# Performance work log

Hardware: AMD Instinct MI355X
Metric: run time of the kernel (lower is better)

## Reference

```python
import jax, jax.numpy as jnp
import numpy as np
import math

DIM = 896
NH = 8
HD = DIM // NH  # 112
B, T, KA_RAW, KT = 64, 8, 64, 512
KA = KA_RAW + 1  # adapter tokens + p conditioning token


def rope_cos_sin(L, hd):
    inv = 1.0 / (10000.0 ** (jnp.arange(0, hd, 2, dtype=jnp.float32) / hd))
    freqs = jnp.arange(L, dtype=jnp.float32)[:, None] * inv[None, :]  # (L, hd/2)
    emb = jnp.concatenate([freqs, freqs], axis=-1)  # (L, hd)
    return jnp.cos(emb), jnp.sin(emb)


def rotate_half(x):
    # interleaved rotation, faithful to the torch code
    x1 = x[..., ::2]
    x2 = x[..., 1::2]
    return jnp.stack((-x2, x1), axis=-1).reshape(x.shape)


def rope_apply(t, cos, sin):
    # cos/sin: (L, hd) broadcast over (B, H, L, hd)
    return t * cos + rotate_half(t) * sin


def heads(t):
    Bb, L, _ = t.shape
    return t.reshape(Bb, L, NH, HD).transpose(0, 2, 1, 3)  # (B, H, L, hd)


def setup_inputs() -> dict:
    key = jax.random.key(0)
    ks = jax.random.split(key, 32)
    s = 0.02
    d = {
        'x': jax.random.normal(ks[0], (B, T, DIM), jnp.float32),
        'h_a': jax.random.normal(ks[1], (B, KA_RAW, DIM), jnp.float32),
        'h_t': jax.random.normal(ks[2], (B, KT, DIM), jnp.float32),
        'p': jax.random.normal(ks[3], (B, 1, DIM), jnp.float32),
    }
    names = ['Wq', 'Wks', 'Wvs', 'Wka', 'Wva', 'Wkt', 'Wvt', 'Wo', 'Wf']
    for i, n in enumerate(names):
        d[n] = s * jax.random.normal(ks[4 + i], (DIM, DIM), jnp.float32)
        d['b' + n[1:]] = s * jax.random.normal(ks[16 + i], (DIM,), jnp.float32)
    d['gate'] = jnp.full((1,), 0.1, jnp.float32)  # nonzero so task branch is active
    d['ln_g'] = jnp.ones((DIM,), jnp.float32)
    d['ln_b'] = jnp.zeros((DIM,), jnp.float32)
    return d


def reference(x, h_a, h_t, p,
              Wq, bq, Wks, bks, Wvs, bvs, Wka, bka, Wva, bva,
              Wkt, bkt, Wvt, bvt, Wo, bo, Wf, bf,
              gate, ln_g, ln_b):
    ratio_g = jnp.tanh(gate)  # (1,)
    h_ad = jnp.concatenate([h_a, p], axis=1)  # (B, KA, C)

    q = heads(x @ Wq + bq)            # (B,H,T,hd)
    k_s = heads(x @ Wks + bks)
    v_s = heads(x @ Wvs + bvs)
    k_a = heads(h_ad @ Wka + bka)     # (B,H,KA,hd)
    v_a = heads(h_ad @ Wva + bva)
    k_t = heads(h_t @ Wkt + bkt)      # (B,H,KT,hd)
    v_t = heads(h_t @ Wvt + bvt)

    cos_m, sin_m = rope_cos_sin(T, HD)
    q = rope_apply(q, cos_m, sin_m)
    k_s = rope_apply(k_s, cos_m, sin_m)
    cos_a, sin_a = rope_cos_sin(KA, HD)
    k_a = rope_apply(k_a, cos_a, sin_a)
    cos_t, sin_t = rope_cos_sin(KT, HD)
    k_t = rope_apply(k_t, cos_t, sin_t)

    s_self = jnp.einsum('bhtd,bhkd->bhtk', q, k_s)
    s_ad = jnp.einsum('bhtd,bhkd->bhtk', q, k_a)
    s_task = jnp.einsum('bhtd,bhkd->bhtk', q, k_t) * ratio_g
    scores = jnp.concatenate([s_self, s_ad, s_task], axis=-1) / math.sqrt(HD)
    w = jax.nn.softmax(scores, axis=-1)  # (B,H,T,T+KA+KT)

    v = jnp.concatenate([v_s, v_a, v_t], axis=2)  # (B,H,T+KA+KT,hd)
    out = jnp.einsum('bhtk,bhkd->bhtd', w, v)
    out = out.transpose(0, 2, 1, 3).reshape(x.shape)  # (B,T,C)
    out = out @ Wo + bo

    y = out + x
    mu = jnp.mean(y, axis=-1, keepdims=True)
    var = jnp.var(y, axis=-1, keepdims=True)
    yn = (y - mu) / jnp.sqrt(var + 1e-5) * ln_g + ln_b
    return jax.nn.relu(yn @ Wf + bf)
```

## Files before the change

kernel.cpp:

```cpp
#include <hip/hip_runtime.h>
#include <hip/hip_bf16.h>
#include <math.h>

#define DIM 896
#define DD  (DIM * DIM)
#define NH 8
#define HD 112
#define BB 64
#define TT 8
#define KA 65
#define KAPAD 4224
#define KT 512
#define NKEYS (TT + KA + KT)

#define EPI_NONE  0
#define EPI_ROPE  1
#define EPI_RESID 2
#define EPI_RELU  3

#define NEG_L2_10K_OVER_56 (-0.2373327285062406f)

#ifndef __has_builtin
#define __has_builtin(x) 0
#endif
#if __has_builtin(__builtin_amdgcn_global_load_lds)
#define HAS_GLL 1
#else
#define HAS_GLL 0
#endif

typedef __attribute__((ext_vector_type(8))) short bf16x8_t;
typedef __attribute__((ext_vector_type(4))) float f32x4_t;

__device__ __forceinline__ short f2bf(float f) {
  unsigned u = __float_as_uint(f);
  u += 0x7fffu + ((u >> 16) & 1u);
  return (short)(u >> 16);
}
__device__ __forceinline__ float bf2f(short s) {
  return __uint_as_float(((unsigned)(unsigned short)s) << 16);
}
__device__ __forceinline__ unsigned cvt_pk_bf16(float lo, float hi) {
  unsigned r;
  asm("v_cvt_pk_bf16_f32 %0, %1, %2" : "=v"(r) : "v"(lo), "v"(hi));
  return r;
}
__device__ __forceinline__ void gll16(const short* g, short* lbase, int lane) {
#if HAS_GLL
  __builtin_amdgcn_global_load_lds(
      (const __attribute__((address_space(1))) unsigned*)g,
      (__attribute__((address_space(3))) unsigned*)lbase, 16, 0, 0);
#else
  *(bf16x8_t*)(lbase + lane * 8) = *(const bf16x8_t*)g;
#endif
}

struct W9 { const float* w[9]; };

__global__ __launch_bounds__(256) void wtrans(W9 ws, short* __restrict__ Wt)
{
  __shared__ float t[32][33];
  const float* W = ws.w[blockIdx.z];
  short* dst = Wt + (size_t)blockIdx.z * DD;
  const int bx = blockIdx.x, by = blockIdx.y;
  const int tx = threadIdx.x & 31, ty = threadIdx.x >> 5;
#pragma unroll
  for (int i = 0; i < 4; ++i)
    t[ty + i * 8][tx] = W[(size_t)(by * 32 + ty + i * 8) * DIM + bx * 32 + tx];
  __syncthreads();
#pragma unroll
  for (int i = 0; i < 4; ++i)
    dst[(size_t)(bx * 32 + ty + i * 8) * DIM + by * 32 + tx] = f2bf(t[tx][ty + i * 8]);
}

__global__ __launch_bounds__(256) void build_had(
    const float* __restrict__ h_a, const float* __restrict__ p,
    short* __restrict__ had)
{
  const int i = blockIdx.x * 256 + threadIdx.x;
  const int total = KAPAD * DIM / 8;
  if (i >= total) return;
  const int c = (i % 112) * 8;
  const int row = i / 112;
  bf16x8_t o;
  if (row >= BB * KA) {
#pragma unroll
    for (int j = 0; j < 8; ++j) o[j] = 0;
  } else {
    const int b = row / KA, j = row % KA;
    const float* src = (j < KA - 1) ? h_a + ((size_t)b * (KA - 1) + j) * DIM + c
                                    : p + (size_t)b * DIM + c;
    const float4 a = *(const float4*)src;
    const float4 d = *(const float4*)(src + 4);
    o[0] = f2bf(a.x); o[1] = f2bf(a.y); o[2] = f2bf(a.z); o[3] = f2bf(a.w);
    o[4] = f2bf(d.x); o[5] = f2bf(d.y); o[6] = f2bf(d.z); o[7] = f2bf(d.w);
  }
  ((bf16x8_t*)had)[i] = o;
}

struct EpiCfg {
  const float* bias[3];
  float* outF[3];
  short* outB[3];
  const float* resid;
  int epi[3];
  int pos_mod[3];
  int row_off;
  int hm[3];
  int hm_L[3];
  int hm_ltot[3];
  int swz;
};

template <bool AF32, bool DOLN>
__device__ __forceinline__ void gemm_body(
    short* As, short* Bs,
    const short* A, const float* Af, const short* Wt,
    const EpiCfg& cfg, int bx, int by,
    const float* smu, const float* srs,
    const float* lngam, const float* lnbet)
{
  const int tid = threadIdx.x;
  const int wave = tid >> 6, lane = tid & 63;
  const int sub = bx / 7;
  const int col0 = (bx % 7) * 128;
  const int row0 = by * 128;
  const int wm = wave >> 1, wn = wave & 1;
  const int lm = lane & 15, lq = lane >> 4;

  const int sr = lane >> 3;
  const int sg = (lane & 7) ^ sr;
  const short* Wg = Wt + (size_t)(sub * DIM + col0 + wave * 32 + sr) * DIM + sg * 8;
  const short* Ag = nullptr;
  if constexpr (!AF32)
    Ag = A + (size_t)(row0 + wave * 32 + sr) * DIM + sg * 8;

  f32x4_t acc[4][4];
#pragma unroll
  for (int i = 0; i < 4; ++i)
#pragma unroll
    for (int j = 0; j < 4; ++j) acc[i][j] = (f32x4_t){0.f, 0.f, 0.f, 0.f};

  for (int k0 = 0; k0 < DIM; k0 += 64) {
    __syncthreads();
    if constexpr (AF32) {
#pragma unroll
      for (int j = 0; j < 4; ++j) {
        const int c = tid + 256 * j;
        const int row = c >> 3, g = c & 7;
        const float* srcp = Af + (size_t)(row0 + row) * DIM + k0 + g * 8;
        const float4 a0 = *(const float4*)srcp;
        const float4 a1 = *(const float4*)(srcp + 4);
        float e[8] = {a0.x, a0.y, a0.z, a0.w, a1.x, a1.y, a1.z, a1.w};
        if constexpr (DOLN) {
          const float mu = smu[row], rs = srs[row];
#pragma unroll
          for (int q = 0; q < 8; ++q) {
            const int k = k0 + g * 8 + q;
            e[q] = (e[q] - mu) * rs * lngam[k] + lnbet[k];
          }
        }
        uint4 w;
        w.x = cvt_pk_bf16(e[0], e[1]); w.y = cvt_pk_bf16(e[2], e[3]);
        w.z = cvt_pk_bf16(e[4], e[5]); w.w = cvt_pk_bf16(e[6], e[7]);
        *(uint4*)&As[row * 64 + ((g ^ (row & 7)) << 3)] = w;
      }
    } else {
#pragma unroll
      for (int j = 0; j < 4; ++j)
        gll16(Ag + (size_t)(j * 8) * DIM + k0, &As[(wave * 32 + j * 8) * 64], lane);
    }
#pragma unroll
    for (int j = 0; j < 4; ++j)
      gll16(Wg + (size_t)(j * 8) * DIM + k0, &Bs[(wave * 32 + j * 8) * 64], lane);
    __syncthreads();

    bf16x8_t afr[4][2], bfr[4][2];
#pragma unroll
    for (int t = 0; t < 4; ++t) {
      const int ra = wm * 64 + t * 16 + lm;
      const int rb = wn * 64 + t * 16 + lm;
      afr[t][0] = *(const bf16x8_t*)&As[ra * 64 + (((lq) ^ (ra & 7)) << 3)];
      afr[t][1] = *(const bf16x8_t*)&As[ra * 64 + (((4 + lq) ^ (ra & 7)) << 3)];
      bfr[t][0] = *(const bf16x8_t*)&Bs[rb * 64 + (((lq) ^ (rb & 7)) << 3)];
      bfr[t][1] = *(const bf16x8_t*)&Bs[rb * 64 + (((4 + lq) ^ (rb & 7)) << 3)];
    }
#pragma unroll
    for (int kk = 0; kk < 2; ++kk)
#pragma unroll
      for (int tm = 0; tm < 4; ++tm)
#pragma unroll
        for (int tn = 0; tn < 4; ++tn)
          acc[tm][tn] = __builtin_amdgcn_mfma_f32_16x16x32_bf16(
              afr[tm][kk], bfr[tn][kk], acc[tm][tn], 0, 0, 0);
  }

  const float* bias = cfg.bias[sub];
  float* outF = cfg.outF[sub];
  short* outB = cfg.outB[sub];
  const int epi = cfg.epi[sub], pm = cfg.pos_mod[sub];
  const int hm = cfg.hm[sub];
  const int L = cfg.hm_L[sub], ltot = cfg.hm_ltot[sub];

  if (hm) {
    int gl[4][4];
#pragma unroll
    for (int tm = 0; tm < 4; ++tm) {
      const int g = cfg.row_off + row0 + wm * 64 + tm * 16 + lq * 4;
      int bq2 = g / L;
      int l = g - bq2 * L;
#pragma unroll
      for (int r = 0; r < 4; ++r) {
        gl[tm][r] = l;
        if (++l == L) { l = 0; ++bq2; }
      }
    }
    short* Cs = As;
    __syncthreads();
#pragma unroll
    for (int tn = 0; tn < 4; ++tn) {
      const int lc = wn * 64 + tn * 16 + lm;
      const int col = col0 + lc;
      const float bv = bias[col];
      float fr = 0.f, sgn = 0.f;
      if (epi == EPI_ROPE) {
        const int d0 = col % HD;
        fr = exp2f((float)(d0 % 56) * NEG_L2_10K_OVER_56);
        sgn = (d0 & 1) ? 1.f : -1.f;
      }
#pragma unroll
      for (int tm = 0; tm < 4; ++tm) {
#pragma unroll
        for (int r = 0; r < 4; ++r) {
          float v = acc[tm][tn][r] + bv;
          if (epi == EPI_ROPE) {
            const float prt = __shfl_xor(v, 1);
            float s, c;
            __sincosf((float)gl[tm][r] * fr, &s, &c);
            v = v * c + sgn * prt * s;
          }
          const int lr = wm * 64 + tm * 16 + lq * 4 + r;
          const int gp = (lc >> 3) ^ (((lr >> 2) & 3) << 1);
          Cs[lr * 128 + gp * 8 + (lc & 7)] = f2bf(v);
        }
      }
    }
    __syncthreads();
#pragma unroll
    for (int i = 0; i < 8; ++i) {
      const int ch = tid + 256 * i;
      const int lr = ch >> 4, g = ch & 15;
      const int phys = g ^ (((lr >> 2) & 3) << 1);
      const bf16x8_t val = *(const bf16x8_t*)&Cs[lr * 128 + phys * 8];
      const int grow = cfg.row_off + row0 + lr;
      const int bq2 = grow / L;
      const int l = grow - bq2 * L;
      const int col = col0 + g * 8;
      const int h = col / HD, d = col - h * HD;
      if (bq2 < BB)
        *(bf16x8_t*)&outB[((size_t)(bq2 * NH + h) * ltot + l) * HD + d] = val;
    }
    return;
  }

#pragma unroll
  for (int tn = 0; tn < 4; ++tn) {
    const int col = col0 + wn * 64 + tn * 16 + lm;
    const float bv = bias[col];
#pragma unroll
    for (int tm = 0; tm < 4; ++tm) {
#pragma unroll
      for (int r = 0; r < 4; ++r) {
        const int grow = cfg.row_off + row0 + wm * 64 + tm * 16 + lq * 4 + r;
        float v = acc[tm][tn][r] + bv;
        if (epi == EPI_RESID) {
          v += cfg.resid[(size_t)grow * DIM + col];
        } else if (epi == EPI_RELU) {
          v = fmaxf(v, 0.f);
        }
        if (outB) outB[(size_t)grow * DIM + col] = f2bf(v);
        else      outF[(size_t)grow * DIM + col] = v;
      }
    }
  }
}

template <bool AF32>
__global__ __launch_bounds__(256) void gemm_bf16(
    const short* __restrict__ A, const float* __restrict__ Af,
    const short* __restrict__ Wt, EpiCfg cfg)
{
  __shared__ __align__(16) short lds[2 * 128 * 64];
  int bx = blockIdx.x, by = blockIdx.y;
  if (cfg.swz) {
    const int nx = gridDim.x;
    const int bid = blockIdx.x + blockIdx.y * nx;
    const int xcd = bid & 7, ixd = bid >> 3;
    const int rpx = gridDim.y >> 3;
    bx = ixd % nx;
    by = xcd * rpx + ixd / nx;
  }
  gemm_body<AF32, false>(lds, lds + 128 * 64, A, Af, Wt, cfg, bx, by,
                         nullptr, nullptr, nullptr, nullptr);
}

__global__ __launch_bounds__(256) void gemm_ffn(
    const float* __restrict__ Y, const float* __restrict__ lng,
    const float* __restrict__ lnb, const short* __restrict__ Wt, EpiCfg cfg)
{
  __shared__ __align__(16) short lds[2 * 128 * 64];
  __shared__ float glds[DIM], blds[DIM];
  __shared__ float smu[128], srs[128];
  const int tid = threadIdx.x;
  const int row0 = blockIdx.y * 128;
  for (int i = tid; i < DIM; i += 256) { glds[i] = lng[i]; blds[i] = lnb[i]; }
  {
    const int r = tid >> 1, h = tid & 1;
    const float* rp = Y + (size_t)(row0 + r) * DIM + h * 448;
    float s = 0.f, q = 0.f;
    for (int i = 0; i < 448; i += 4) {
      const float4 v = *(const float4*)(rp + i);
      s += v.x + v.y + v.z + v.w;
      q = fmaf(v.x, v.x, fmaf(v.y, v.y, fmaf(v.z, v.z, fmaf(v.w, v.w, q))));
    }
    s += __shfl_xor(s, 1);
    q += __shfl_xor(q, 1);
    if (h == 0) {
      const float mu = s * (1.f / DIM);
      const float var = q * (1.f / DIM) - mu * mu;
      smu[r] = mu;
      srs[r] = 1.f / sqrtf(var + 1e-5f);
    }
  }
  __syncthreads();
  gemm_body<true, true>(lds, lds + 128 * 64, nullptr, Y, Wt, cfg,
                        blockIdx.x, blockIdx.y, smu, srs, glds, blds);
}

#define SCP 10

__global__ __launch_bounds__(1024, 8) void attn_kernel(
    const short* __restrict__ q, const short* __restrict__ kall,
    const short* __restrict__ vall, const float* __restrict__ gate,
    short* __restrict__ out)
{
  __shared__ __align__(16) float qs[TT * HD];
  __shared__ __align__(16) float sc[NKEYS * SCP];
  __shared__ float red[TT * TT * HD];
  __shared__ float isum[TT];
  const int tid = threadIdx.x;
  const int bh = blockIdx.x;
  const float scale = 0.09449111825230681f;
  const float rg = tanhf(gate[0]);

  if (tid < TT * HD) qs[tid] = bf2f(q[(size_t)bh * (TT * HD) + tid]);
  __syncthreads();

  if (tid < NKEYS) {
    const int k = tid;
    const short* kp = kall + ((size_t)bh * NKEYS + k) * HD;
    float dot[TT] = {};
    for (int d8 = 0; d8 < HD; d8 += 8) {
      const bf16x8_t kv8 = *(const bf16x8_t*)(kp + d8);
      float kf[8];
#pragma unroll
      for (int j = 0; j < 8; ++j) kf[j] = bf2f(kv8[j]);
#pragma unroll
      for (int t = 0; t < TT; ++t) {
        const float4 qa = *(const float4*)&qs[t * HD + d8];
        const float4 qb4 = *(const float4*)&qs[t * HD + d8 + 4];
        dot[t] = fmaf(qa.x, kf[0], dot[t]);
        dot[t] = fmaf(qa.y, kf[1], dot[t]);
        dot[t] = fmaf(qa.z, kf[2], dot[t]);
        dot[t] = fmaf(qa.w, kf[3], dot[t]);
        dot[t] = fmaf(qb4.x, kf[4], dot[t]);
        dot[t] = fmaf(qb4.y, kf[5], dot[t]);
        dot[t] = fmaf(qb4.z, kf[6], dot[t]);
        dot[t] = fmaf(qb4.w, kf[7], dot[t]);
      }
    }
    const float s = (k >= TT + KA) ? scale * rg : scale;
#pragma unroll
    for (int t = 0; t < TT; ++t) sc[k * SCP + t] = dot[t] * s;
  }
  __syncthreads();

  const int wave = tid >> 6, lane = tid & 63;
  if (wave < TT) {
    const int t = wave;
    float m = -1e30f;
    for (int k = lane; k < NKEYS; k += 64) m = fmaxf(m, sc[k * SCP + t]);
#pragma unroll
    for (int o = 32; o >= 1; o >>= 1) m = fmaxf(m, __shfl_xor(m, o));
    float sum = 0.f;
    for (int k = lane; k < NKEYS; k += 64) {
      const float e = expf(sc[k * SCP + t] - m);
      sc[k * SCP + t] = e;
      sum += e;
    }
#pragma unroll
    for (int o = 32; o >= 1; o >>= 1) sum += __shfl_xor(sum, o);
    if (lane == 0) isum[t] = 1.f / sum;
  }
  __syncthreads();

  if (tid < TT * HD) {
    const int g = tid / HD, d = tid - (tid / HD) * HD;
    const int kb = (g * NKEYS) / TT, ke = ((g + 1) * NKEYS) / TT;
    const short* vp = vall + (size_t)bh * (NKEYS * HD) + d;
    float acc[TT] = {};
    for (int k = kb; k < ke; ++k) {
      const float vv = bf2f(vp[(size_t)k * HD]);
      const float2 s0 = *(const float2*)&sc[k * SCP];
      const float2 s1 = *(const float2*)&sc[k * SCP + 2];
      const float2 s2 = *(const float2*)&sc[k * SCP + 4];
      const float2 s3 = *(const float2*)&sc[k * SCP + 6];
      acc[0] = fmaf(s0.x, vv, acc[0]);
      acc[1] = fmaf(s0.y, vv, acc[1]);
      acc[2] = fmaf(s1.x, vv, acc[2]);
      acc[3] = fmaf(s1.y, vv, acc[3]);
      acc[4] = fmaf(s2.x, vv, acc[4]);
      acc[5] = fmaf(s2.y, vv, acc[5]);
      acc[6] = fmaf(s3.x, vv, acc[6]);
      acc[7] = fmaf(s3.y, vv, acc[7]);
    }
#pragma unroll
    for (int t = 0; t < TT; ++t) red[(g * TT + t) * HD + d] = acc[t];
  }
  __syncthreads();

  if (tid < TT * HD) {
    const int t = tid / HD, d = tid - (tid / HD) * HD;
    float a = 0.f;
#pragma unroll
    for (int g = 0; g < TT; ++g) a += red[(g * TT + t) * HD + d];
    out[((size_t)(bh >> 3) * TT + t) * DIM + (bh & 7) * HD + d] = f2bf(a * isum[t]);
  }
}

extern "C" void kernel_launch(void* const* d_in, const int* in_sizes, int n_in,
                              void* d_out, int out_size, void* d_ws, size_t ws_size,
                              hipStream_t stream)
{
  const float* x   = (const float*)d_in[0];
  const float* h_a = (const float*)d_in[1];
  const float* h_t = (const float*)d_in[2];
  const float* p   = (const float*)d_in[3];
  const float* Wq  = (const float*)d_in[4];  const float* bq  = (const float*)d_in[5];
  const float* Wks = (const float*)d_in[6];  const float* bks = (const float*)d_in[7];
  const float* Wvs = (const float*)d_in[8];  const float* bvs = (const float*)d_in[9];
  const float* Wka = (const float*)d_in[10]; const float* bka = (const float*)d_in[11];
  const float* Wva = (const float*)d_in[12]; const float* bva = (const float*)d_in[13];
  const float* Wkt = (const float*)d_in[14]; const float* bkt = (const float*)d_in[15];
  const float* Wvt = (const float*)d_in[16]; const float* bvt = (const float*)d_in[17];
  const float* Wo  = (const float*)d_in[18]; const float* bo  = (const float*)d_in[19];
  const float* Wf  = (const float*)d_in[20]; const float* bf_ = (const float*)d_in[21];
  const float* gate = (const float*)d_in[22];
  const float* ln_g = (const float*)d_in[23];
  const float* ln_b = (const float*)d_in[24];

  const size_t SZ_HAD = (size_t)KAPAD * DIM * 2;
  const size_t SZ_SM  = (size_t)BB * TT * DIM * 2;
  const size_t SZ_KV  = (size_t)BB * NH * NKEYS * HD * 2;
  const size_t SZ_WT  = (size_t)9 * DD * 2;
  const size_t needed = SZ_HAD + SZ_SM * 2 + SZ_KV * 2 + SZ_WT
                        + (size_t)BB * TT * DIM * 4;
  if (ws_size < needed) return;

  char* wsp = (char*)d_ws;
  short* hadb = (short*)wsp; wsp += SZ_HAD;
  short* qb   = (short*)wsp; wsp += SZ_SM;
  short* kall = (short*)wsp; wsp += SZ_KV;
  short* vall = (short*)wsp; wsp += SZ_KV;
  short* WtA  = (short*)wsp; wsp += SZ_WT;
  short* attn_outb = (short*)wsp; wsp += SZ_SM;
  float* yb   = (float*)wsp; wsp += (size_t)BB * TT * DIM * 4;

  dim3 blk(256);

  W9 w9; const float* Ws[9] = {Wq, Wks, Wvs, Wka, Wva, Wkt, Wvt, Wo, Wf};
  for (int i = 0; i < 9; ++i) w9.w[i] = Ws[i];
  wtrans<<<dim3(28, 28, 9), blk, 0, stream>>>(w9, WtA);

  build_had<<<(KAPAD * DIM / 8 + 255) / 256, blk, 0, stream>>>(h_a, p, hadb);

  {
    EpiCfg c = {};
    c.bias[0] = bq;  c.outB[0] = qb;   c.epi[0] = EPI_ROPE; c.pos_mod[0] = TT;
    c.hm[0] = 1; c.hm_L[0] = TT; c.hm_ltot[0] = TT;
    c.bias[1] = bks; c.outB[1] = kall; c.epi[1] = EPI_ROPE; c.pos_mod[1] = TT;
    c.hm[1] = 1; c.hm_L[1] = TT; c.hm_ltot[1] = NKEYS;
    c.bias[2] = bvs; c.outB[2] = vall; c.epi[2] = EPI_NONE; c.pos_mod[2] = 1;
    c.hm[2] = 1; c.hm_L[2] = TT; c.hm_ltot[2] = NKEYS;
    gemm_bf16<true><<<dim3(21, BB * TT / 128), blk, 0, stream>>>(nullptr, x, WtA, c);
  }
  {
    EpiCfg c = {};
    c.bias[0] = bka; c.outB[0] = kall + (size_t)TT * HD; c.epi[0] = EPI_ROPE;
    c.pos_mod[0] = KA; c.hm[0] = 1; c.hm_L[0] = KA; c.hm_ltot[0] = NKEYS;
    c.bias[1] = bva; c.outB[1] = vall + (size_t)TT * HD; c.epi[1] = EPI_NONE;
    c.pos_mod[1] = 1; c.hm[1] = 1; c.hm_L[1] = KA; c.hm_ltot[1] = NKEYS;
    gemm_bf16<false><<<dim3(14, KAPAD / 128), blk, 0, stream>>>(
        hadb, nullptr, WtA + (size_t)3 * DD, c);
  }
  {
    EpiCfg c = {};
    c.bias[0] = bkt; c.outB[0] = kall + (size_t)(TT + KA) * HD; c.epi[0] = EPI_ROPE;
    c.pos_mod[0] = KT; c.hm[0] = 1; c.hm_L[0] = KT; c.hm_ltot[0] = NKEYS;
    c.bias[1] = bvt; c.outB[1] = vall + (size_t)(TT + KA) * HD; c.epi[1] = EPI_NONE;
    c.pos_mod[1] = 1; c.hm[1] = 1; c.hm_L[1] = KT; c.hm_ltot[1] = NKEYS;
    c.row_off = 0;
    c.swz = 1;
    gemm_bf16<true><<<dim3(14, BB * KT / 128), blk, 0, stream>>>(
        nullptr, h_t, WtA + (size_t)5 * DD, c);
  }

  attn_kernel<<<BB * NH, dim3(1024), 0, stream>>>(qb, kall, vall, gate, attn_outb);

  {
    EpiCfg c = {};
    c.bias[0] = bo; c.outF[0] = yb; c.epi[0] = EPI_RESID; c.pos_mod[0] = 1;
    c.resid = x;
    gemm_bf16<false><<<dim3(7, BB * TT / 128), blk, 0, stream>>>(
        attn_outb, nullptr, WtA + (size_t)7 * DD, c);
  }
  {
    EpiCfg c = {};
    c.bias[0] = bf_; c.outF[0] = (float*)d_out; c.epi[0] = EPI_RELU; c.pos_mod[0] = 1;
    gemm_ffn<<<dim3(7, BB * TT / 128), blk, 0, stream>>>(
        yb, ln_g, ln_b, WtA + (size_t)8 * DD, c);
  }
}
```

Baseline: 695.9 us.

## Add software-pipelined GEMM with register-prefetched fp32 A and triple-buffered weights

Adds a new gemm_t kernel for the fp32-input projections (QKV self and task K/V). It prefetches fp32 A tiles into registers two steps ahead, converts them to bf16 into double-buffered LDS, and triple-buffers weight tiles via async global-to-LDS loads. It uses explicit vmcnt waits and a single barrier per k-step. The goal is to overlap global loads with MFMA work and remove the two-barrier serial load/compute loop, at the cost of more LDS (80KB) and register pressure, which may lower occupancy.

```diff
diff --git a/kernel.cpp b/kernel.cpp
--- a/kernel.cpp
+++ b/kernel.cpp
@@ -112,6 +112,215 @@
   int swz;
 };
 
+__device__ __forceinline__ void compute_step(
+    const short* As, const short* Bs, f32x4_t (&acc)[4][4],
+    int wm, int wn, int lm, int lq)
+{
+  bf16x8_t afr[4][2], bfr[4][2];
+#pragma unroll
+  for (int t = 0; t < 4; ++t) {
+    const int ra = wm * 64 + t * 16 + lm;
+    const int rb = wn * 64 + t * 16 + lm;
+    afr[t][0] = *(const bf16x8_t*)&As[ra * 64 + (((lq) ^ (ra & 7)) << 3)];
+    afr[t][1] = *(const bf16x8_t*)&As[ra * 64 + (((4 + lq) ^ (ra & 7)) << 3)];
+    bfr[t][0] = *(const bf16x8_t*)&Bs[rb * 64 + (((lq) ^ (rb & 7)) << 3)];
+    bfr[t][1] = *(const bf16x8_t*)&Bs[rb * 64 + (((4 + lq) ^ (rb & 7)) << 3)];
+  }
+#pragma unroll
+  for (int kk = 0; kk < 2; ++kk)
+#pragma unroll
+    for (int tm = 0; tm < 4; ++tm)
+#pragma unroll
+      for (int tn = 0; tn < 4; ++tn)
+        acc[tm][tn] = __builtin_amdgcn_mfma_f32_16x16x32_bf16(
+            afr[tm][kk], bfr[tn][kk], acc[tm][tn], 0, 0, 0);
+}
+
+__device__ __forceinline__ void epilogue_hm(
+    short* Cs, f32x4_t (&acc)[4][4], const EpiCfg& cfg,
+    int bx, int by, int wm, int wn, int lm, int lq, int tid)
+{
+  const int sub = bx / 7;
+  const int col0 = (bx % 7) * 128;
+  const int row0 = by * 128;
+  const float* bias = cfg.bias[sub];
+  short* outB = cfg.outB[sub];
+  const int epi = cfg.epi[sub];
+  const int L = cfg.hm_L[sub], ltot = cfg.hm_ltot[sub];
+  int gl[4][4];
+#pragma unroll
+  for (int tm = 0; tm < 4; ++tm) {
+    const int g = cfg.row_off + row0 + wm * 64 + tm * 16 + lq * 4;
+    int bq2 = g / L;
+    int l = g - bq2 * L;
+#pragma unroll
+    for (int r = 0; r < 4; ++r) {
+      gl[tm][r] = l;
+      if (++l == L) { l = 0; ++bq2; }
+    }
+  }
+  __syncthreads();
+#pragma unroll
+  for (int tn = 0; tn < 4; ++tn) {
+    const int lc = wn * 64 + tn * 16 + lm;
+    const int col = col0 + lc;
+    const float bv = bias[col];
+    float fr = 0.f, sgn = 0.f;
+    if (epi == EPI_ROPE) {
+      const int d0 = col % HD;
+      fr = exp2f((float)(d0 % 56) * NEG_L2_10K_OVER_56);
+      sgn = (d0 & 1) ? 1.f : -1.f;
+    }
+#pragma unroll
+    for (int tm = 0; tm < 4; ++tm) {
+#pragma unroll
+      for (int r = 0; r < 4; ++r) {
+        float v = acc[tm][tn][r] + bv;
+        if (epi == EPI_ROPE) {
+          const float prt = __shfl_xor(v, 1);
+          float s, c;
+          __sincosf((float)gl[tm][r] * fr, &s, &c);
+          v = v * c + sgn * prt * s;
+        }
+        const int lr = wm * 64 + tm * 16 + lq * 4 + r;
+        const int gp = (lc >> 3) ^ (((lr >> 2) & 3) << 1);
+        Cs[lr * 128 + gp * 8 + (lc & 7)] = f2bf(v);
+      }
+    }
+  }
+  __syncthreads();
+#pragma unroll
+  for (int i = 0; i < 8; ++i) {
+    const int ch = tid + 256 * i;
+    const int lr = ch >> 4, g = ch & 15;
+    const int phys = g ^ (((lr >> 2) & 3) << 1);
+    const bf16x8_t val = *(const bf16x8_t*)&Cs[lr * 128 + phys * 8];
+    const int grow = cfg.row_off + row0 + lr;
+    const int bq2 = grow / L;
+    const int l = grow - bq2 * L;
+    const int col = col0 + g * 8;
+    const int h = col / HD, d = col - h * HD;
+    if (bq2 < BB)
+      *(bf16x8_t*)&outB[((size_t)(bq2 * NH + h) * ltot + l) * HD + d] = val;
+  }
+}
+
+struct ASet { float4 v[8]; };
+
+__device__ __forceinline__ void a_issue(ASet& s, const float* Af, int row0,
+                                        int k0, int tid)
+{
+#pragma unroll
+  for (int j = 0; j < 4; ++j) {
+    const int c = tid + 256 * j;
+    const int row = c >> 3, g = c & 7;
+    const float* p = Af + (size_t)(row0 + row) * DIM + k0 + g * 8;
+    s.v[2 * j]     = *(const float4*)p;
+    s.v[2 * j + 1] = *(const float4*)(p + 4);
+  }
+}
+__device__ __forceinline__ void a_commit(const ASet& s, short* As, int tid)
+{
+#pragma unroll
+  for (int j = 0; j < 4; ++j) {
+    const int c = tid + 256 * j;
+    const int row = c >> 3, g = c & 7;
+    const float4 a0 = s.v[2 * j], a1 = s.v[2 * j + 1];
+    uint4 w;
+    w.x = cvt_pk_bf16(a0.x, a0.y); w.y = cvt_pk_bf16(a0.z, a0.w);
+    w.z = cvt_pk_bf16(a1.x, a1.y); w.w = cvt_pk_bf16(a1.z, a1.w);
+    *(uint4*)&As[row * 64 + ((g ^ (row & 7)) << 3)] = w;
+  }
+}
+__device__ __forceinline__ void w_issue(const short* Wg, int k0, short* Wbuf,
+                                        int wave, int lane)
+{
+#pragma unroll
+  for (int j = 0; j < 4; ++j)
+    gll16(Wg + (size_t)(j * 8) * DIM + k0, &Wbuf[(wave * 32 + j * 8) * 64], lane);
+}
+
+__global__ __launch_bounds__(256) void gemm_t(
+    const float* __restrict__ Af, const short* __restrict__ Wt, EpiCfg cfg)
+{
+  __shared__ __align__(16) short lds[5 * 128 * 64];
+  short* ldsA = lds;
+  short* ldsW = lds + 2 * 8192;
+  const int tid = threadIdx.x;
+  const int wave = tid >> 6, lane = tid & 63;
+
+  int bx = blockIdx.x, by = blockIdx.y;
+  if (cfg.swz) {
+    const int nx = gridDim.x;
+    const int bid = blockIdx.x + blockIdx.y * nx;
+    const int xcd = bid & 7, ixd = bid >> 3;
+    const int rpx = gridDim.y >> 3;
+    bx = ixd % nx;
+    by = xcd * rpx + ixd / nx;
+  }
+  const int sub = bx / 7;
+  const int col0 = (bx % 7) * 128;
+  const int row0 = by * 128;
+  const int wm = wave >> 1, wn = wave & 1;
+  const int lm = lane & 15, lq = lane >> 4;
+
+  const int sr = lane >> 3;
+  const int sg = (lane & 7) ^ sr;
+  const short* Wg = Wt + (size_t)(sub * DIM + col0 + wave * 32 + sr) * DIM + sg * 8;
+
+  f32x4_t acc[4][4];
+#pragma unroll
+  for (int i = 0; i < 4; ++i)
+#pragma unroll
+    for (int j = 0; j < 4; ++j) acc[i][j] = (f32x4_t){0.f, 0.f, 0.f, 0.f};
+
+  ASet sA, sB;
+
+  w_issue(Wg, 0, ldsW, wave, lane);
+  a_issue(sA, Af, row0, 0, tid);
+  w_issue(Wg, 64, ldsW + 8192, wave, lane);
+  a_issue(sB, Af, row0, 64, tid);
+  asm volatile("s_waitcnt vmcnt(12)" ::: "memory");
+  a_commit(sA, ldsA, tid);
+  asm volatile("s_waitcnt lgkmcnt(0)" ::: "memory");
+  __builtin_amdgcn_s_barrier();
+  asm volatile("" ::: "memory");
+
+#define TSTEP(k, Sissue, Scommit, VMS)                                         \
+  {                                                                            \
+    if ((k) + 2 < 14) {                                                        \
+      w_issue(Wg, ((k) + 2) * 64, ldsW + (((k) + 2) % 3) * 8192, wave, lane);  \
+      a_issue(Sissue, Af, row0, ((k) + 2) * 64, tid);                          \
+    }                                                                          \
+    asm volatile("s_waitcnt " VMS ::: "memory");                               \
+    if ((k) + 1 < 14)                                                          \
+      a_commit(Scommit, ldsA + (((k) + 1) & 1) * 8192, tid);                   \
+    compute_step(ldsA + ((k) & 1) * 8192, ldsW + ((k) % 3) * 8192,             \
+                 acc, wm, wn, lm, lq);                                         \
+    asm volatile("s_waitcnt lgkmcnt(0)" ::: "memory");                         \
+    __builtin_amdgcn_s_barrier();                                              \
+    asm volatile("" ::: "memory");                                             \
+  }
+
+  TSTEP(0,  sA, sB, "vmcnt(12)")
+  TSTEP(1,  sB, sA, "vmcnt(12)")
+  TSTEP(2,  sA, sB, "vmcnt(12)")
+  TSTEP(3,  sB, sA, "vmcnt(12)")
+  TSTEP(4,  sA, sB, "vmcnt(12)")
+  TSTEP(5,  sB, sA, "vmcnt(12)")
+  TSTEP(6,  sA, sB, "vmcnt(12)")
+  TSTEP(7,  sB, sA, "vmcnt(12)")
+  TSTEP(8,  sA, sB, "vmcnt(12)")
+  TSTEP(9,  sB, sA, "vmcnt(12)")
+  TSTEP(10, sA, sB, "vmcnt(12)")
+  TSTEP(11, sB, sA, "vmcnt(12)")
+  TSTEP(12, sA, sB, "vmcnt(0)")
+  TSTEP(13, sB, sA, "vmcnt(0)")
+#undef TSTEP
+
+  epilogue_hm(lds, acc, cfg, bx, by, wm, wn, lm, lq, tid);
+}
+
 template <bool AF32, bool DOLN>
 __device__ __forceinline__ void gemm_body(
     short* As, short* Bs,
@@ -175,94 +384,19 @@
       gll16(Wg + (size_t)(j * 8) * DIM + k0, &Bs[(wave * 32 + j * 8) * 64], lane);
     __syncthreads();
 
-    bf16x8_t afr[4][2], bfr[4][2];
-#pragma unroll
-    for (int t = 0; t < 4; ++t) {
-      const int ra = wm * 64 + t * 16 + lm;
-      const int rb = wn * 64 + t * 16 + lm;
-      afr[t][0] = *(const bf16x8_t*)&As[ra * 64 + (((lq) ^ (ra & 7)) << 3)];
-      afr[t][1] = *(const bf16x8_t*)&As[ra * 64 + (((4 + lq) ^ (ra & 7)) << 3)];
-      bfr[t][0] = *(const bf16x8_t*)&Bs[rb * 64 + (((lq) ^ (rb & 7)) << 3)];
-      bfr[t][1] = *(const bf16x8_t*)&Bs[rb * 64 + (((4 + lq) ^ (rb & 7)) << 3)];
-    }
-#pragma unroll
-    for (int kk = 0; kk < 2; ++kk)
-#pragma unroll
-      for (int tm = 0; tm < 4; ++tm)
-#pragma unroll
-        for (int tn = 0; tn < 4; ++tn)
-          acc[tm][tn] = __builtin_amdgcn_mfma_f32_16x16x32_bf16(
-              afr[tm][kk], bfr[tn][kk], acc[tm][tn], 0, 0, 0);
+    compute_step(As, Bs, acc, wm, wn, lm, lq);
+  }
+
+  const int hm = cfg.hm[sub];
+  if (hm) {
+    epilogue_hm(As, acc, cfg, bx, by, wm, wn, lm, lq, tid);
+    return;
   }
 
   const float* bias = cfg.bias[sub];
   float* outF = cfg.outF[sub];
   short* outB = cfg.outB[sub];
-  const int epi = cfg.epi[sub], pm = cfg.pos_mod[sub];
-  const int hm = cfg.hm[sub];
-  const int L = cfg.hm_L[sub], ltot = cfg.hm_ltot[sub];
-
-  if (hm) {
-    int gl[4][4];
-#pragma unroll
-    for (int tm = 0; tm < 4; ++tm) {
-      const int g = cfg.row_off + row0 + wm * 64 + tm * 16 + lq * 4;
-      int bq2 = g / L;
-      int l = g - bq2 * L;
-#pragma unroll
-      for (int r = 0; r < 4; ++r) {
-        gl[tm][r] = l;
-        if (++l == L) { l = 0; ++bq2; }
-      }
-    }
-    short* Cs = As;
-    __syncthreads();
-#pragma unroll
-    for (int tn = 0; tn < 4; ++tn) {
-      const int lc = wn * 64 + tn * 16 + lm;
-      const int col = col0 + lc;
-      const float bv = bias[col];
-      float fr = 0.f, sgn = 0.f;
-      if (epi == EPI_ROPE) {
-        const int d0 = col % HD;
-        fr = exp2f((float)(d0 % 56) * NEG_L2_10K_OVER_56);
-        sgn = (d0 & 1) ? 1.f : -1.f;
-      }
-#pragma unroll
-      for (int tm = 0; tm < 4; ++tm) {
-#pragma unroll
-        for (int r = 0; r < 4; ++r) {
-          float v = acc[tm][tn][r] + bv;
-          if (epi == EPI_ROPE) {
-            const float prt = __shfl_xor(v, 1);
-            float s, c;
-            __sincosf((float)gl[tm][r] * fr, &s, &c);
-            v = v * c + sgn * prt * s;
-          }
-          const int lr = wm * 64 + tm * 16 + lq * 4 + r;
-          const int gp = (lc >> 3) ^ (((lr >> 2) & 3) << 1);
-          Cs[lr * 128 + gp * 8 + (lc & 7)] = f2bf(v);
-        }
-      }
-    }
-    __syncthreads();
-#pragma unroll
-    for (int i = 0; i < 8; ++i) {
-      const int ch = tid + 256 * i;
-      const int lr = ch >> 4, g = ch & 15;
-      const int phys = g ^ (((lr >> 2) & 3) << 1);
-      const bf16x8_t val = *(const bf16x8_t*)&Cs[lr * 128 + phys * 8];
-      const int grow = cfg.row_off + row0 + lr;
-      const int bq2 = grow / L;
-      const int l = grow - bq2 * L;
-      const int col = col0 + g * 8;
-      const int h = col / HD, d = col - h * HD;
-      if (bq2 < BB)
-        *(bf16x8_t*)&outB[((size_t)(bq2 * NH + h) * ltot + l) * HD + d] = val;
-    }
-    return;
-  }
-
+  const int epi = cfg.epi[sub];
 #pragma unroll
   for (int tn = 0; tn < 4; ++tn) {
     const int col = col0 + wn * 64 + tn * 16 + lm;
@@ -285,23 +419,12 @@
   }
 }
 
-template <bool AF32>
 __global__ __launch_bounds__(256) void gemm_bf16(
-    const short* __restrict__ A, const float* __restrict__ Af,
-    const short* __restrict__ Wt, EpiCfg cfg)
+    const short* __restrict__ A, const short* __restrict__ Wt, EpiCfg cfg)
 {
   __shared__ __align__(16) short lds[2 * 128 * 64];
-  int bx = blockIdx.x, by = blockIdx.y;
-  if (cfg.swz) {
-    const int nx = gridDim.x;
-    const int bid = blockIdx.x + blockIdx.y * nx;
-    const int xcd = bid & 7, ixd = bid >> 3;
-    const int rpx = gridDim.y >> 3;
-    bx = ixd % nx;
-    by = xcd * rpx + ixd / nx;
-  }
-  gemm_body<AF32, false>(lds, lds + 128 * 64, A, Af, Wt, cfg, bx, by,
-                         nullptr, nullptr, nullptr, nullptr);
+  gemm_body<false, false>(lds, lds + 128 * 64, A, nullptr, Wt, cfg,
+                          blockIdx.x, blockIdx.y, nullptr, nullptr, nullptr, nullptr);
 }
 
 __global__ __launch_bounds__(256) void gemm_ffn(
@@ -492,7 +615,7 @@
     c.hm[1] = 1; c.hm_L[1] = TT; c.hm_ltot[1] = NKEYS;
     c.bias[2] = bvs; c.outB[2] = vall; c.epi[2] = EPI_NONE; c.pos_mod[2] = 1;
     c.hm[2] = 1; c.hm_L[2] = TT; c.hm_ltot[2] = NKEYS;
-    gemm_bf16<true><<<dim3(21, BB * TT / 128), blk, 0, stream>>>(nullptr, x, WtA, c);
+    gemm_t<<<dim3(21, BB * TT / 128), blk, 0, stream>>>(x, WtA, c);
   }
   {
     EpiCfg c = {};
@@ -500,8 +623,8 @@
     c.pos_mod[0] = KA; c.hm[0] = 1; c.hm_L[0] = KA; c.hm_ltot[0] = NKEYS;
     c.bias[1] = bva; c.outB[1] = vall + (size_t)TT * HD; c.epi[1] = EPI_NONE;
     c.pos_mod[1] = 1; c.hm[1] = 1; c.hm_L[1] = KA; c.hm_ltot[1] = NKEYS;
-    gemm_bf16<false><<<dim3(14, KAPAD / 128), blk, 0, stream>>>(
-        hadb, nullptr, WtA + (size_t)3 * DD, c);
+    gemm_bf16<<<dim3(14, KAPAD / 128), blk, 0, stream>>>(
+        hadb, WtA + (size_t)3 * DD, c);
   }
   {
     EpiCfg c = {};
@@ -511,8 +634,8 @@
     c.pos_mod[1] = 1; c.hm[1] = 1; c.hm_L[1] = KT; c.hm_ltot[1] = NKEYS;
     c.row_off = 0;
     c.swz = 1;
-    gemm_bf16<true><<<dim3(14, BB * KT / 128), blk, 0, stream>>>(
-        nullptr, h_t, WtA + (size_t)5 * DD, c);
+    gemm_t<<<dim3(14, BB * KT / 128), blk, 0, stream>>>(
+        h_t, WtA + (size_t)5 * DD, c);
   }
 
   attn_kernel<<<BB * NH, dim3(1024), 0, stream>>>(qb, kall, vall, gate, attn_outb);
@@ -521,8 +644,8 @@
     EpiCfg c = {};
     c.bias[0] = bo; c.outF[0] = yb; c.epi[0] = EPI_RESID; c.pos_mod[0] = 1;
     c.resid = x;
-    gemm_bf16<false><<<dim3(7, BB * TT / 128), blk, 0, stream>>>(
-        attn_outb, nullptr, WtA + (size_t)7 * DD, c);
+    gemm_bf16<<<dim3(7, BB * TT / 128), blk, 0, stream>>>(
+        attn_outb, WtA + (size_t)7 * DD, c);
   }
   {
     EpiCfg c = {};
```

New measurement: 643.7 us. 1.08x faster.
